# Optimization experiments

Hardware: AMD Instinct MI355X
Metric: run time of the kernel (lower is better)

The kernel has to match this reference:

```python
import jax, jax.numpy as jnp
import numpy as np

N_NODES = 50000
N_EDGES = 800000
N_GRAPHS = 1024
BN_EPS = 1e-5

def _linear_params(key, fan_in, fan_out):
    k1, k2 = jax.random.split(key)
    lim = 1.0 / np.sqrt(fan_in)
    w = jax.random.uniform(k1, (fan_in, fan_out), jnp.float32, -lim, lim)
    b = jax.random.uniform(k2, (fan_out,), jnp.float32, -lim, lim)
    return w, b


def setup_inputs() -> dict:
    key = jax.random.key(0)
    ks = jax.random.split(key, 16)
    x = jax.random.normal(ks[0], (N_NODES, 114), jnp.float32)
    edge_index = jax.random.randint(ks[1], (2, N_EDGES), 0, N_NODES, jnp.int64)
    batch = jnp.sort(jax.random.randint(ks[2], (N_NODES,), 0, N_GRAPHS, jnp.int64))
    w1a, b1a = _linear_params(ks[3], 114, 198)
    w1b, b1b = _linear_params(ks[4], 198, 198)
    w2a, b2a = _linear_params(ks[5], 198, 64)
    w2b, b2b = _linear_params(ks[6], 64, 64)
    w3a, b3a = _linear_params(ks[7], 64, 32)
    w3b, b3b = _linear_params(ks[8], 32, 32)
    fw1, fb1 = _linear_params(ks[9], 32, 16)
    fw2, fb2 = _linear_params(ks[10], 16, 8)
    ow, ob = _linear_params(ks[11], 8, 2)
    g1 = jnp.ones((198,), jnp.float32); be1 = jnp.zeros((198,), jnp.float32)
    g2 = jnp.ones((64,), jnp.float32); be2 = jnp.zeros((64,), jnp.float32)
    g3 = jnp.ones((32,), jnp.float32); be3 = jnp.zeros((32,), jnp.float32)
    return dict(x=x, edge_index=edge_index, batch=batch,
                w1a=w1a, b1a=b1a, w1b=w1b, b1b=b1b, g1=g1, be1=be1,
                w2a=w2a, b2a=b2a, w2b=w2b, b2b=b2b, g2=g2, be2=be2,
                w3a=w3a, b3a=b3a, w3b=w3b, b3b=b3b, g3=g3, be3=be3,
                fw1=fw1, fb1=fb1, fw2=fw2, fb2=fb2, ow=ow, ob=ob)


def _gin_conv(x, src, dst, wa, ba, wb, bb):
    # GINConv, eps=0: h_i = MLP((1+eps)*x_i + sum_{j->i} x_j)
    agg = jax.ops.segment_sum(x[src], dst, num_segments=N_NODES)
    h = x + agg
    h = jax.nn.relu(h @ wa + ba) @ wb + bb
    return h


def _batchnorm(h, gamma, beta):
    # training-mode BN over the node axis (biased variance, as torch)
    mean = jnp.mean(h, axis=0)
    var = jnp.var(h, axis=0)
    return (h - mean) * jax.lax.rsqrt(var + BN_EPS) * gamma + beta


def reference(x, edge_index, batch,
              w1a, b1a, w1b, b1b, g1, be1,
              w2a, b2a, w2b, b2b, g2, be2,
              w3a, b3a, w3b, b3b, g3, be3,
              fw1, fb1, fw2, fb2, ow, ob):
    src, dst = edge_index[0], edge_index[1]
    h = jax.nn.relu(_gin_conv(x, src, dst, w1a, b1a, w1b, b1b))
    h = _batchnorm(h, g1, be1)
    h = jax.nn.relu(_gin_conv(h, src, dst, w2a, b2a, w2b, b2b))
    h = _batchnorm(h, g2, be2)
    h = jax.nn.relu(_gin_conv(h, src, dst, w3a, b3a, w3b, b3b))
    h = _batchnorm(h, g3, be3)
    g = jax.ops.segment_sum(h, batch, num_segments=N_GRAPHS)  # global_add_pool
    g = jax.nn.relu(g @ fw1 + fb1)
    g = jax.nn.relu(g @ fw2 + fb2)
    return g @ ow + ob
```

## Files before the change

kernel.cpp:

```cpp
#include <hip/hip_runtime.h>

#define NODES  50000
#define EDGES  800000
#define GRAPHS 1024
#define P      200

#define SCAN_BLK 256
#define SCAN_NB  ((NODES + SCAN_BLK - 1) / SCAN_BLK)

typedef __attribute__((ext_vector_type(8))) short short8v;
typedef __attribute__((ext_vector_type(4))) short short4v;
typedef __attribute__((ext_vector_type(4))) float f32x4;

__device__ __forceinline__ ushort f2bf(float f) {
    uint u = __float_as_uint(f);
    u = u + 0x7FFFu + ((u >> 16) & 1u);
    return (ushort)(u >> 16);
}

__global__ void hist_kernel(const int* __restrict__ dst, int* __restrict__ deg) {
    int e = blockIdx.x * blockDim.x + threadIdx.x;
    if (e < EDGES) atomicAdd(&deg[dst[e]], 1);
}

__global__ void scan_part(const int* __restrict__ deg, int* __restrict__ part) {
    __shared__ int sh[SCAN_BLK];
    int t = threadIdx.x;
    int n = blockIdx.x * SCAN_BLK + t;
    sh[t] = (n < NODES) ? deg[n] : 0;
    __syncthreads();
    for (int off = SCAN_BLK / 2; off > 0; off >>= 1) {
        if (t < off) sh[t] += sh[t + off];
        __syncthreads();
    }
    if (t == 0) part[blockIdx.x] = sh[0];
}

__global__ void scan_scan(int* __restrict__ part) {
    __shared__ int sh[SCAN_BLK];
    int t = threadIdx.x;
    int v = (t < SCAN_NB) ? part[t] : 0;
    sh[t] = v;
    __syncthreads();
    for (int off = 1; off < SCAN_BLK; off <<= 1) {
        int u = 0;
        if (t >= off) u = sh[t - off];
        __syncthreads();
        if (t >= off) sh[t] += u;
        __syncthreads();
    }
    if (t < SCAN_NB) part[t] = sh[t] - v;
}

__global__ void scan_expand(const int* __restrict__ deg, const int* __restrict__ part,
                            int* __restrict__ rowstart, int* __restrict__ cursor) {
    __shared__ int sh[SCAN_BLK];
    int t = threadIdx.x;
    int n = blockIdx.x * SCAN_BLK + t;
    int v = (n < NODES) ? deg[n] : 0;
    sh[t] = v;
    __syncthreads();
    for (int off = 1; off < SCAN_BLK; off <<= 1) {
        int u = 0;
        if (t >= off) u = sh[t - off];
        __syncthreads();
        if (t >= off) sh[t] += u;
        __syncthreads();
    }
    int excl = sh[t] - v + part[blockIdx.x];
    if (n < NODES) {
        rowstart[n] = excl;
        cursor[n]   = excl;
        if (n == NODES - 1) rowstart[NODES] = excl + v;
    }
}

__global__ void scatter_kernel(const int* __restrict__ src, const int* __restrict__ dst,
                               int* __restrict__ cursor, int* __restrict__ csrc) {
    int e = blockIdx.x * blockDim.x + threadIdx.x;
    if (e < EDGES) {
        int p = atomicAdd(&cursor[dst[e]], 1);
        csrc[p] = src[e];
    }
}

__global__ void pad_w_mfma(const float* __restrict__ W, int K, int N, int NCH, int CT,
                           ushort* __restrict__ out) {
    int s = blockIdx.x * blockDim.x + threadIdx.x;
    int half = NCH * CT * 512;
    if (s >= 2 * half) return;
    int h = s / half;
    int r = s % half;
    int j = r & 7, col = (r >> 3) & 15, kg = (r >> 7) & 3;
    int rest = r >> 9;
    int ct = rest % CT, c = rest / CT;
    int k = c * 32 + kg * 8 + j;
    int n = ct * 16 + col;
    float v = (k < K && n < N) ? W[k * N + n] : 0.0f;
    ushort hi = f2bf(v);
    if (h == 0) out[s] = hi;
    else {
        float hf = __uint_as_float(((uint)hi) << 16);
        out[s] = f2bf(v - hf);
    }
}

template<int D>
__global__ void csr_agg(const float* __restrict__ feat, int fpitch,
                        const int* __restrict__ rowstart, const int* __restrict__ csrc,
                        float* __restrict__ agg, int opitch) {
    int wid  = (blockIdx.x * blockDim.x + threadIdx.x) >> 6;
    int lane = threadIdx.x & 63;
    if (wid >= NODES) return;
    constexpr int NI  = (D + 63) / 64;
    constexpr int UNR = 8;
    float s[NI];
#pragma unroll
    for (int i = 0; i < NI; i++) s[i] = 0.0f;
    const int r0 = rowstart[wid], r1 = rowstart[wid + 1];
    for (int base = r0; base < r1; base += 64) {
        const int myidx = (base + lane < r1) ? csrc[base + lane] : 0;
        const int cnt = min(64, r1 - base);
        int t = 0;
        for (; t + UNR <= cnt; t += UNR) {
            const float* p[UNR];
#pragma unroll
            for (int u = 0; u < UNR; u++)
                p[u] = feat + (size_t)__shfl(myidx, t + u) * fpitch;
            float v[UNR][NI];
#pragma unroll
            for (int u = 0; u < UNR; u++)
#pragma unroll
                for (int i = 0; i < NI; i++) {
                    int c = lane + 64 * i;
                    if (c < D) v[u][i] = p[u][c];
                }
#pragma unroll
            for (int i = 0; i < NI; i++) {
                int c = lane + 64 * i;
                if (c < D) {
                    float acc = 0.0f;
#pragma unroll
                    for (int u = 0; u < UNR; u++) acc += v[u][i];
                    s[i] += acc;
                }
            }
        }
        for (; t < cnt; t++) {
            const float* fp2 = feat + (size_t)__shfl(myidx, t) * fpitch;
#pragma unroll
            for (int i = 0; i < NI; i++) {
                int c = lane + 64 * i;
                if (c < D) s[i] += fp2[c];
            }
        }
    }
    float* ap = agg + (size_t)wid * opitch;
#pragma unroll
    for (int i = 0; i < NI; i++) {
        int c = lane + 64 * i;
        if (c < D) ap[c] = s[i];
    }
}

__launch_bounds__(256)
__global__ void gemm_fused_l1(const float* __restrict__ X,
                              const float* __restrict__ A2,
                              const ushort* __restrict__ WF1,
                              const float* __restrict__ B1,
                              const ushort* __restrict__ WF2,
                              const float* __restrict__ B2,
                              float* __restrict__ OUT,
                              float* __restrict__ gsum, float* __restrict__ gsq) {
    constexpr int K1   = 114;
    constexpr int NCH1 = 4;
    constexpr int NCH2 = 7;
    constexpr int CT   = 16;
    constexpr int CTW  = 4;
    constexpr int NN   = 198;

    __shared__ __align__(16) ushort A_lds[2][2][2][4][16][8];
    __shared__ __align__(16) ushort M_lds[2][NCH2][2][4][16][8];
    __shared__ float shSum[256];
    __shared__ float shSq [256];

    const int tid  = threadIdx.x;
    const int lane = tid & 63;
    const int wv   = tid >> 6;
    const int node0 = blockIdx.x * 32;

    for (int n = tid; n < 256; n += 256) { shSum[n] = 0.0f; shSq[n] = 0.0f; }

    const int sr  = tid >> 3;
    const int sc4 = (tid & 7) * 4;
    const int skg = sc4 >> 3;
    const int sj0 = sc4 & 7;
    const int gn  = node0 + sr;
    const size_t fstride1 = (size_t)NCH1 * CT * 512;
    const size_t fstride2 = (size_t)NCH2 * CT * 512;

    float xv[4];
    float a2v[4];

    auto loadA = [&](int c) {
        const int k0 = c * 32 + sc4;
#pragma unroll
        for (int j = 0; j < 4; j++) {
            int gk = k0 + j;
            bool ok = (gn < NODES && gk < K1);
            xv[j]  = ok ? X[(size_t)gn * K1 + gk] : 0.0f;
            a2v[j] = ok ? A2[(size_t)gn * P + gk] : 0.0f;
        }
    };
    auto cvtStore = [&](int buf, int c) {
        const int k0 = c * 32 + sc4;
        short4v hv, lv;
#pragma unroll
        for (int j = 0; j < 4; j++) {
            int gk = k0 + j;
            float t = 0.0f;
            if (gn < NODES && gk < K1) t = xv[j] + a2v[j];
            ushort h = f2bf(t);
            float hf = __uint_as_float(((uint)h) << 16);
            ushort l = f2bf(t - hf);
            hv[j] = (short)h; lv[j] = (short)l;
        }
        *(short4v*)&A_lds[buf][0][sr >> 4][skg][sr & 15][sj0] = hv;
        *(short4v*)&A_lds[buf][1][sr >> 4][skg][sr & 15][sj0] = lv;
    };

    f32x4 acc1[2][CTW] = {};
    loadA(0);
    cvtStore(0, 0);
    __syncthreads();

    const int kg = lane >> 4, rw = lane & 15;
#pragma unroll
    for (int c = 0; c < NCH1; c++) {
        const int buf = c & 1;
        if (c + 1 < NCH1) loadA(c + 1);

        short8v ah[2], al[2];
#pragma unroll
        for (int rt = 0; rt < 2; rt++) {
            ah[rt] = *(const short8v*)&A_lds[buf][0][rt][kg][rw][0];
            al[rt] = *(const short8v*)&A_lds[buf][1][rt][kg][rw][0];
        }
        const size_t fb0 = ((size_t)(c * CT + wv * CTW)) * 512 + (size_t)lane * 8;
        short8v wh = *(const short8v*)(WF1 + fb0);
        short8v wl = *(const short8v*)(WF1 + fstride1 + fb0);
#pragma unroll
        for (int t = 0; t < CTW; t++) {
            short8v nwh, nwl;
            if (t + 1 < CTW) {
                const size_t fb = fb0 + (size_t)(t + 1) * 512;
                nwh = *(const short8v*)(WF1 + fb);
                nwl = *(const short8v*)(WF1 + fstride1 + fb);
            }
            __builtin_amdgcn_s_setprio(1);
#pragma unroll
            for (int rt = 0; rt < 2; rt++) {
                acc1[rt][t] = __builtin_amdgcn_mfma_f32_16x16x32_bf16(ah[rt], wh, acc1[rt][t], 0, 0, 0);
                acc1[rt][t] = __builtin_amdgcn_mfma_f32_16x16x32_bf16(al[rt], wh, acc1[rt][t], 0, 0, 0);
                acc1[rt][t] = __builtin_amdgcn_mfma_f32_16x16x32_bf16(ah[rt], wl, acc1[rt][t], 0, 0, 0);
            }
            __builtin_amdgcn_s_setprio(0);
            if (t + 1 < CTW) { wh = nwh; wl = nwl; }
        }
        if (c + 1 < NCH1) cvtStore((c + 1) & 1, c + 1);
        __syncthreads();
    }

    const int mg = lane >> 4, colb = lane & 15;
#pragma unroll
    for (int t = 0; t < CTW; t++) {
        const int ct = wv * CTW + t;
        if (ct >= 14) continue;
        const int n = ct * 16 + colb;
        const float bn = (n < NN) ? B1[n] : 0.0f;
        const int c2 = n >> 5, kg2 = (n >> 3) & 3, j2 = n & 7;
#pragma unroll
        for (int rt = 0; rt < 2; rt++) {
#pragma unroll
            for (int j = 0; j < 4; j++) {
                float vv = fmaxf(acc1[rt][t][j] + bn, 0.0f);
                if (n >= NN) vv = 0.0f;
                ushort h = f2bf(vv);
                float hf = __uint_as_float(((uint)h) << 16);
                ushort l = f2bf(vv - hf);
                int row = mg * 4 + j;
                M_lds[0][c2][rt][kg2][row][j2] = h;
                M_lds[1][c2][rt][kg2][row][j2] = l;
            }
        }
    }
    __syncthreads();

    f32x4 acc2[2][CTW] = {};
#pragma unroll
    for (int c = 0; c < NCH2; c++) {
        short8v ah[2], al[2];
#pragma unroll
        for (int rt = 0; rt < 2; rt++) {
            ah[rt] = *(const short8v*)&M_lds[0][c][rt][kg][rw][0];
            al[rt] = *(const short8v*)&M_lds[1][c][rt][kg][rw][0];
        }
        const size_t fb0 = ((size_t)(c * CT + wv * CTW)) * 512 + (size_t)lane * 8;
        short8v wh = *(const short8v*)(WF2 + fb0);
        short8v wl = *(const short8v*)(WF2 + fstride2 + fb0);
#pragma unroll
        for (int t = 0; t < CTW; t++) {
            short8v nwh, nwl;
            if (t + 1 < CTW) {
                const size_t fb = fb0 + (size_t)(t + 1) * 512;
                nwh = *(const short8v*)(WF2 + fb);
                nwl = *(const short8v*)(WF2 + fstride2 + fb);
            }
            __builtin_amdgcn_s_setprio(1);
#pragma unroll
            for (int rt = 0; rt < 2; rt++) {
                acc2[rt][t] = __builtin_amdgcn_mfma_f32_16x16x32_bf16(ah[rt], wh, acc2[rt][t], 0, 0, 0);
                acc2[rt][t] = __builtin_amdgcn_mfma_f32_16x16x32_bf16(al[rt], wh, acc2[rt][t], 0, 0, 0);
                acc2[rt][t] = __builtin_amdgcn_mfma_f32_16x16x32_bf16(ah[rt], wl, acc2[rt][t], 0, 0, 0);
            }
            __builtin_amdgcn_s_setprio(0);
            if (t + 1 < CTW) { wh = nwh; wl = nwl; }
        }
    }

#pragma unroll
    for (int t = 0; t < CTW; t++) {
        const int ct = wv * CTW + t;
        const int n = ct * 16 + colb;
        const float bn = (n < NN) ? B2[n] : 0.0f;
        float psum = 0.0f, psq = 0.0f;
#pragma unroll
        for (int rt = 0; rt < 2; rt++) {
#pragma unroll
            for (int j = 0; j < 4; j++) {
                int m = node0 + rt * 16 + mg * 4 + j;
                float vv = fmaxf(acc2[rt][t][j] + bn, 0.0f);
                if (m < NODES && n < NN) {
                    OUT[(size_t)m * P + n] = vv;
                    psum += vv; psq += vv * vv;
                }
            }
        }
        if (n < NN) {
            atomicAdd(&shSum[n], psum);
            atomicAdd(&shSq[n], psq);
        }
    }
    __syncthreads();
    for (int n = tid; n < NN; n += 256) {
        atomicAdd(&gsum[n], shSum[n]);
        atomicAdd(&gsq[n], shSq[n]);
    }
}

template<int K, int N, bool ADD2, bool STATS, bool BNX, bool PRE, bool ACT>
__launch_bounds__(256)
__global__ void gemm_mfma(const float* __restrict__ X, int xpitch,
                          const float* __restrict__ A2, int apitch,
                          const ushort* __restrict__ WF,
                          const float* __restrict__ B,
                          const float* __restrict__ PREB,
                          const float* __restrict__ scale, const float* __restrict__ shift,
                          float* __restrict__ OUT, int opitch,
                          float* __restrict__ gsum, float* __restrict__ gsq) {
    constexpr int KP  = ((K + 31) / 32) * 32;
    constexpr int NCH = KP / 32;
    constexpr int NP  = ((N + 63) / 64) * 64;
    constexpr int CT  = NP / 16;
    constexpr int CTW = CT / 4;
    static_assert(CT % 4 == 0, "col tiles must split across 4 waves");

    __shared__ __align__(16) ushort A_lds[2][2][2][4][16][8];
    __shared__ float shSum[STATS ? NP : 4];
    __shared__ float shSq [STATS ? NP : 4];

    const int tid  = threadIdx.x;
    const int lane = tid & 63;
    const int wv   = tid >> 6;
    const int node0 = blockIdx.x * 32;

    if (STATS) {
        for (int n = tid; n < NP; n += 256) { shSum[n] = 0.0f; shSq[n] = 0.0f; }
    }

    f32x4 acc[2][CTW] = {};

    const int sr  = tid >> 3;
    const int sc4 = (tid & 7) * 4;
    const int skg = sc4 >> 3;
    const int sj0 = sc4 & 7;
    const int gn  = node0 + sr;
    const size_t fstride = (size_t)NCH * CT * 512;

    float xvA[4], xvB[4];
    float a2vA[ADD2 ? 4 : 1], a2vB[ADD2 ? 4 : 1];

    auto loadA_A = [&](int c) {
        const int k0 = c * 32 + sc4;
#pragma unroll
        for (int j = 0; j < 4; j++) {
            int gk = k0 + j;
            bool ok = (gn < NODES && gk < K);
            xvA[j] = ok ? X[(size_t)gn * xpitch + gk] : 0.0f;
            if (ADD2) a2vA[j] = ok ? A2[(size_t)gn * apitch + gk] : 0.0f;
        }
    };
    auto loadA_B = [&](int c) {
        const int k0 = c * 32 + sc4;
#pragma unroll
        for (int j = 0; j < 4; j++) {
            int gk = k0 + j;
            bool ok = (gn < NODES && gk < K);
            xvB[j] = ok ? X[(size_t)gn * xpitch + gk] : 0.0f;
            if (ADD2) a2vB[j] = ok ? A2[(size_t)gn * apitch + gk] : 0.0f;
        }
    };
    auto cvtCore = [&](int buf, int c, const float* xv, const float* a2v) {
        const int k0 = c * 32 + sc4;
        short4v hv, lv;
#pragma unroll
        for (int j = 0; j < 4; j++) {
            int gk = k0 + j;
            float t = 0.0f;
            if (gn < NODES && gk < K) {
                t = xv[j];
                if (BNX) t = fmaf(t, scale[gk], shift[gk]);
                if (ADD2) t += a2v[j];
                if (PRE)  t = fmaxf(t + PREB[gk], 0.0f);
            }
            ushort h = f2bf(t);
            float hf = __uint_as_float(((uint)h) << 16);
            ushort l = f2bf(t - hf);
            hv[j] = (short)h; lv[j] = (short)l;
        }
        *(short4v*)&A_lds[buf][0][sr >> 4][skg][sr & 15][sj0] = hv;
        *(short4v*)&A_lds[buf][1][sr >> 4][skg][sr & 15][sj0] = lv;
    };

    loadA_A(0);
    if (NCH > 1) loadA_B(1);
    cvtCore(0, 0, xvA, ADD2 ? a2vA : xvA);
    __syncthreads();

    const int kg = lane >> 4, rw = lane & 15;
#pragma unroll
    for (int c = 0; c < NCH; c++) {
        const int buf = c & 1;
        if (c + 2 < NCH) {
            if ((c & 1) == 0) loadA_A(c + 2);
            else              loadA_B(c + 2);
        }

        short8v ah[2], al[2];
#pragma unroll
        for (int rt = 0; rt < 2; rt++) {
            ah[rt] = *(const short8v*)&A_lds[buf][0][rt][kg][rw][0];
            al[rt] = *(const short8v*)&A_lds[buf][1][rt][kg][rw][0];
        }

        const size_t fb0 = ((size_t)(c * CT + wv * CTW)) * 512 + (size_t)lane * 8;
        short8v wh = *(const short8v*)(WF + fb0);
        short8v wl = *(const short8v*)(WF + fstride + fb0);
#pragma unroll
        for (int t = 0; t < CTW; t++) {
            short8v nwh, nwl;
            if (t + 1 < CTW) {
                const size_t fb = fb0 + (size_t)(t + 1) * 512;
                nwh = *(const short8v*)(WF + fb);
                nwl = *(const short8v*)(WF + fstride + fb);
            }
            __builtin_amdgcn_s_setprio(1);
#pragma unroll
            for (int rt = 0; rt < 2; rt++) {
                acc[rt][t] = __builtin_amdgcn_mfma_f32_16x16x32_bf16(ah[rt], wh, acc[rt][t], 0, 0, 0);
                acc[rt][t] = __builtin_amdgcn_mfma_f32_16x16x32_bf16(al[rt], wh, acc[rt][t], 0, 0, 0);
                acc[rt][t] = __builtin_amdgcn_mfma_f32_16x16x32_bf16(ah[rt], wl, acc[rt][t], 0, 0, 0);
            }
            __builtin_amdgcn_s_setprio(0);
            if (t + 1 < CTW) { wh = nwh; wl = nwl; }
        }

        if (c + 1 < NCH) {
            if (((c + 1) & 1) == 0) cvtCore((c + 1) & 1, c + 1, xvA, ADD2 ? a2vA : xvA);
            else                    cvtCore((c + 1) & 1, c + 1, xvB, ADD2 ? a2vB : xvB);
        }
        __syncthreads();
    }

    const int mg = lane >> 4, colb = lane & 15;
#pragma unroll
    for (int t = 0; t < CTW; t++) {
        const int ct = wv * CTW + t;
        const int n = ct * 16 + colb;
        const float bn = (ACT && n < N) ? B[n] : 0.0f;
        float psum = 0.0f, psq = 0.0f;
#pragma unroll
        for (int rt = 0; rt < 2; rt++) {
#pragma unroll
            for (int j = 0; j < 4; j++) {
                int m = node0 + rt * 16 + mg * 4 + j;
                float vv = ACT ? fmaxf(acc[rt][t][j] + bn, 0.0f) : acc[rt][t][j];
                if (m < NODES && n < N) {
                    OUT[(size_t)m * opitch + n] = vv;
                    if (STATS) { psum += vv; psq += vv * vv; }
                }
            }
        }
        if (STATS && n < N) {
            atomicAdd(&shSum[n], psum);
            atomicAdd(&shSq[n], psq);
        }
    }
    if (STATS) {
        __syncthreads();
        for (int n = tid; n < N; n += 256) {
            atomicAdd(&gsum[n], shSum[n]);
            atomicAdd(&gsq[n], shSq[n]);
        }
    }
}

template<int N>
__global__ void bn_finalize(const float* __restrict__ sum, const float* __restrict__ sq,
                            const float* __restrict__ gamma, const float* __restrict__ beta,
                            float* __restrict__ scale, float* __restrict__ shift) {
    int n = threadIdx.x;
    if (n < N) {
        float mean = sum[n] * (1.0f / NODES);
        float var  = sq[n] * (1.0f / NODES) - mean * mean;
        var = var < 0.0f ? 0.0f : var;
        float sc = gamma[n] * rsqrtf(var + 1e-5f);
        scale[n] = sc;
        shift[n] = beta[n] - mean * sc;
    }
}

__global__ void pool_kernel(const float* __restrict__ h, const int* __restrict__ batch,
                            const float* __restrict__ scale, const float* __restrict__ shift,
                            float* __restrict__ g) {
    int idx = blockIdx.x * blockDim.x + threadIdx.x;
    if (idx >= NODES * 32) return;
    int n = idx >> 5, f = idx & 31;
    float v = fmaf(h[(size_t)n * 32 + f], scale[f], shift[f]);
    atomicAdd(&g[batch[n] * 32 + f], v);
}

__global__ void head_kernel(const float* __restrict__ g,
                            const float* __restrict__ fw1, const float* __restrict__ fb1,
                            const float* __restrict__ fw2, const float* __restrict__ fb2,
                            const float* __restrict__ ow, const float* __restrict__ ob,
                            float* __restrict__ out) {
    int gi = blockIdx.x * blockDim.x + threadIdx.x;
    if (gi >= GRAPHS) return;
    float v[32];
#pragma unroll
    for (int k = 0; k < 32; k++) v[k] = g[gi * 32 + k];
    float a1[16];
#pragma unroll
    for (int o = 0; o < 16; o++) {
        float s = fb1[o];
#pragma unroll
        for (int k = 0; k < 32; k++) s = fmaf(v[k], fw1[k * 16 + o], s);
        a1[o] = s > 0.0f ? s : 0.0f;
    }
    float a2[8];
#pragma unroll
    for (int o = 0; o < 8; o++) {
        float s = fb2[o];
#pragma unroll
        for (int k = 0; k < 16; k++) s = fmaf(a1[k], fw2[k * 8 + o], s);
        a2[o] = s > 0.0f ? s : 0.0f;
    }
#pragma unroll
    for (int o = 0; o < 2; o++) {
        float s = ob[o];
#pragma unroll
        for (int k = 0; k < 8; k++) s = fmaf(a2[k], ow[k * 2 + o], s);
        out[gi * 2 + o] = s;
    }
}

extern "C" void kernel_launch(void* const* d_in, const int* in_sizes, int n_in,
                              void* d_out, int out_size, void* d_ws, size_t ws_size,
                              hipStream_t stream) {
    const float* x     = (const float*)d_in[0];
    const int*   ei    = (const int*)d_in[1];
    const int*   batch = (const int*)d_in[2];
    const float *w1a = (const float*)d_in[3],  *b1a = (const float*)d_in[4];
    const float *w1b = (const float*)d_in[5],  *b1b = (const float*)d_in[6];
    const float *g1  = (const float*)d_in[7],  *be1 = (const float*)d_in[8];
    const float *w2a = (const float*)d_in[9],  *b2a = (const float*)d_in[10];
    const float *w2b = (const float*)d_in[11], *b2b = (const float*)d_in[12];
    const float *g2  = (const float*)d_in[13], *be2 = (const float*)d_in[14];
    const float *w3a = (const float*)d_in[15], *b3a = (const float*)d_in[16];
    const float *w3b = (const float*)d_in[17], *b3b = (const float*)d_in[18];
    const float *g3  = (const float*)d_in[19], *be3 = (const float*)d_in[20];
    const float *fw1 = (const float*)d_in[21], *fb1 = (const float*)d_in[22];
    const float *fw2 = (const float*)d_in[23], *fb2 = (const float*)d_in[24];
    const float *ow  = (const float*)d_in[25], *ob  = (const float*)d_in[26];
    const int* src = ei;
    const int* dst = ei + EDGES;

    float* ws    = (float*)d_ws;
    float* b0    = ws;
    float* b1    = ws + (size_t)NODES * P;
    float* Y2    = b1;
    float* AG2   = b1 + (size_t)NODES * 64;
    float* Y3    = b1;
    float* AG3   = b1 + (size_t)NODES * 32;
    float* SUM   = ws + (size_t)2 * NODES * P;
    float* SQ    = SUM + 256;
    float* SCALE = SUM + 512;
    float* SHIFT = SUM + 768;
    float* G     = SUM + 1024;
    int*   deg      = (int*)(G + GRAPHS * 32);
    int*   rowstart = deg + NODES;
    int*   cursor   = rowstart + NODES + 1;
    int*   part     = cursor + NODES;
    int*   csrc     = part + 256;
    uintptr_t wfp = ((uintptr_t)(csrc + EDGES) + 15) & ~(uintptr_t)15;
    ushort* WF1 = (ushort*)wfp;
    ushort* WF2 = WF1 + 65536;
    ushort* WF3 = WF2 + 114688;
    ushort* WF4 = WF3 + 28672;
    ushort* WF5 = WF4 + 8192;
    ushort* WF6 = WF5 + 8192;
    float* out = (float*)d_out;

    const int GBR = (NODES + 31) / 32;
    const int AB = (NODES * 64 + 255) / 256;
    const int EB = (EDGES + 255) / 256;

    pad_w_mfma<<<(65536 + 255) / 256, 256, 0, stream>>>(w1a, 114, 198, 4, 16, WF1);
    pad_w_mfma<<<(114688 + 255) / 256, 256, 0, stream>>>(w1b, 198, 198, 7, 16, WF2);
    pad_w_mfma<<<(28672 + 255) / 256, 256, 0, stream>>>(w2a, 198, 64, 7, 4, WF3);
    pad_w_mfma<<<(8192 + 255) / 256, 256, 0, stream>>>(w2b, 64, 64, 2, 4, WF4);
    pad_w_mfma<<<(8192 + 255) / 256, 256, 0, stream>>>(w3a, 64, 32, 2, 4, WF5);
    pad_w_mfma<<<(4096 + 255) / 256, 256, 0, stream>>>(w3b, 32, 32, 1, 4, WF6);

    hipMemsetAsync(deg, 0, NODES * sizeof(int), stream);
    hist_kernel<<<EB, 256, 0, stream>>>(dst, deg);
    scan_part<<<SCAN_NB, SCAN_BLK, 0, stream>>>(deg, part);
    scan_scan<<<1, SCAN_BLK, 0, stream>>>(part);
    scan_expand<<<SCAN_NB, SCAN_BLK, 0, stream>>>(deg, part, rowstart, cursor);
    scatter_kernel<<<EB, 256, 0, stream>>>(src, dst, cursor, csrc);

    csr_agg<114><<<AB, 256, 0, stream>>>(x, 114, rowstart, csrc, b0, P);
    hipMemsetAsync(SUM, 0, 512 * sizeof(float), stream);
    gemm_fused_l1<<<GBR, 256, 0, stream>>>(x, b0, WF1, b1a, WF2, b1b, b0, SUM, SQ);
    bn_finalize<198><<<1, 256, 0, stream>>>(SUM, SQ, g1, be1, SCALE, SHIFT);

    gemm_mfma<198, 64, false, false, true, false, false><<<GBR, 256, 0, stream>>>(
        b0, P, nullptr, 0, WF3, nullptr, nullptr, SCALE, SHIFT, Y2, 64, nullptr, nullptr);
    csr_agg<64><<<AB, 256, 0, stream>>>(Y2, 64, rowstart, csrc, AG2, 64);
    hipMemsetAsync(SUM, 0, 512 * sizeof(float), stream);
    gemm_mfma<64, 64, true, true, false, true, true><<<GBR, 256, 0, stream>>>(
        Y2, 64, AG2, 64, WF4, b2b, b2a, nullptr, nullptr, b0, 64, SUM, SQ);
    bn_finalize<64><<<1, 256, 0, stream>>>(SUM, SQ, g2, be2, SCALE, SHIFT);

    gemm_mfma<64, 32, false, false, true, false, false><<<GBR, 256, 0, stream>>>(
        b0, 64, nullptr, 0, WF5, nullptr, nullptr, SCALE, SHIFT, Y3, 32, nullptr, nullptr);
    csr_agg<32><<<AB, 256, 0, stream>>>(Y3, 32, rowstart, csrc, AG3, 32);
    hipMemsetAsync(SUM, 0, 512 * sizeof(float), stream);
    gemm_mfma<32, 32, true, true, false, true, true><<<GBR, 256, 0, stream>>>(
        Y3, 32, AG3, 32, WF6, b3b, b3a, nullptr, nullptr, b0, 32, SUM, SQ);
    bn_finalize<32><<<1, 256, 0, stream>>>(SUM, SQ, g3, be3, SCALE, SHIFT);

    hipMemsetAsync(G, 0, GRAPHS * 32 * sizeof(float), stream);
    pool_kernel<<<(NODES * 32 + 255) / 256, 256, 0, stream>>>(b0, batch, SCALE, SHIFT, G);
    head_kernel<<<(GRAPHS + 255) / 256, 256, 0, stream>>>(G, fw1, fb1, fw2, fb2, ow, ob, out);
}
```

Before: 452.6 us.

## Fuse pooling into last GEMM, merge weight padding and memsets, vectorize aggregation

Global add pooling moves into the final GIN GEMM epilogue. It accumulates the raw post-ReLU activations per graph by atomics, and the head applies the BN affine algebraically using per-graph node counts computed in the histogram kernel. This removes the separate pool kernel and the write of the final layer's activations. The six weight-padding launches become one kernel, and the memsets are merged into a single contiguous zeroing with separate stat buffers per layer. The 114-wide aggregation is rewritten to use float2 loads. Per-element atomics in the GEMM epilogue may contend on graph rows.

After: 436.9 us. 1.04x faster.

```diff
diff --git a/kernel.cpp b/kernel.cpp
--- a/kernel.cpp
+++ b/kernel.cpp
@@ -18,9 +18,11 @@
     return (ushort)(u >> 16);
 }
 
-__global__ void hist_kernel(const int* __restrict__ dst, int* __restrict__ deg) {
+__global__ void hist_kernel(const int* __restrict__ dst, int* __restrict__ deg,
+                            const int* __restrict__ batch, int* __restrict__ cnt) {
     int e = blockIdx.x * blockDim.x + threadIdx.x;
     if (e < EDGES) atomicAdd(&deg[dst[e]], 1);
+    if (e < NODES) atomicAdd(&cnt[batch[e]], 1);
 }
 
 __global__ void scan_part(const int* __restrict__ deg, int* __restrict__ part) {
@@ -84,13 +86,24 @@
     }
 }
 
-__global__ void pad_w_mfma(const float* __restrict__ W, int K, int N, int NCH, int CT,
-                           ushort* __restrict__ out) {
+__global__ void pad_all(const float* __restrict__ w1a, const float* __restrict__ w1b,
+                        const float* __restrict__ w2a, const float* __restrict__ w2b,
+                        const float* __restrict__ w3a, const float* __restrict__ w3b,
+                        ushort* __restrict__ WF1, ushort* __restrict__ WF2,
+                        ushort* __restrict__ WF3, ushort* __restrict__ WF4,
+                        ushort* __restrict__ WF5, ushort* __restrict__ WF6) {
     int s = blockIdx.x * blockDim.x + threadIdx.x;
+    const float* W; ushort* out; int K, N, NCH, CT, base;
+    if      (s < 65536)  { W = w1a; out = WF1; K = 114; N = 198; NCH = 4; CT = 16; base = 0; }
+    else if (s < 180224) { W = w1b; out = WF2; K = 198; N = 198; NCH = 7; CT = 16; base = 65536; }
+    else if (s < 208896) { W = w2a; out = WF3; K = 198; N = 64;  NCH = 7; CT = 4;  base = 180224; }
+    else if (s < 217088) { W = w2b; out = WF4; K = 64;  N = 64;  NCH = 2; CT = 4;  base = 208896; }
+    else if (s < 225280) { W = w3a; out = WF5; K = 64;  N = 32;  NCH = 2; CT = 4;  base = 217088; }
+    else if (s < 229376) { W = w3b; out = WF6; K = 32;  N = 32;  NCH = 1; CT = 4;  base = 225280; }
+    else return;
+    int idx = s - base;
     int half = NCH * CT * 512;
-    if (s >= 2 * half) return;
-    int h = s / half;
-    int r = s % half;
+    int h = idx / half, r = idx % half;
     int j = r & 7, col = (r >> 3) & 15, kg = (r >> 7) & 3;
     int rest = r >> 9;
     int ct = rest % CT, c = rest / CT;
@@ -98,10 +111,10 @@
     int n = ct * 16 + col;
     float v = (k < K && n < N) ? W[k * N + n] : 0.0f;
     ushort hi = f2bf(v);
-    if (h == 0) out[s] = hi;
+    if (h == 0) out[idx] = hi;
     else {
         float hf = __uint_as_float(((uint)hi) << 16);
-        out[s] = f2bf(v - hf);
+        out[idx] = f2bf(v - hf);
     }
 }
 
@@ -112,54 +125,64 @@
     int wid  = (blockIdx.x * blockDim.x + threadIdx.x) >> 6;
     int lane = threadIdx.x & 63;
     if (wid >= NODES) return;
-    constexpr int NI  = (D + 63) / 64;
+    const int r0 = rowstart[wid], r1 = rowstart[wid + 1];
     constexpr int UNR = 8;
-    float s[NI];
-#pragma unroll
-    for (int i = 0; i < NI; i++) s[i] = 0.0f;
-    const int r0 = rowstart[wid], r1 = rowstart[wid + 1];
-    for (int base = r0; base < r1; base += 64) {
-        const int myidx = (base + lane < r1) ? csrc[base + lane] : 0;
-        const int cnt = min(64, r1 - base);
-        int t = 0;
-        for (; t + UNR <= cnt; t += UNR) {
-            const float* p[UNR];
-#pragma unroll
-            for (int u = 0; u < UNR; u++)
-                p[u] = feat + (size_t)__shfl(myidx, t + u) * fpitch;
-            float v[UNR][NI];
-#pragma unroll
-            for (int u = 0; u < UNR; u++)
-#pragma unroll
-                for (int i = 0; i < NI; i++) {
-                    int c = lane + 64 * i;
-                    if (c < D) v[u][i] = p[u][c];
+    if constexpr (D == 114) {
+        const bool act = lane < 57;
+        float sx = 0.0f, sy = 0.0f;
+        for (int base = r0; base < r1; base += 64) {
+            const int myidx = (base + lane < r1) ? csrc[base + lane] : 0;
+            const int cnt = min(64, r1 - base);
+            int t = 0;
+            for (; t + UNR <= cnt; t += UNR) {
+                const float2* p[UNR];
+#pragma unroll
+                for (int u = 0; u < UNR; u++)
+                    p[u] = (const float2*)(feat + (size_t)__shfl(myidx, t + u) * fpitch);
+                float2 v[UNR];
+#pragma unroll
+                for (int u = 0; u < UNR; u++) if (act) v[u] = p[u][lane];
+                if (act) {
+                    float ax = 0.0f, ay = 0.0f;
+#pragma unroll
+                    for (int u = 0; u < UNR; u++) { ax += v[u].x; ay += v[u].y; }
+                    sx += ax; sy += ay;
                 }
-#pragma unroll
-            for (int i = 0; i < NI; i++) {
-                int c = lane + 64 * i;
-                if (c < D) {
+            }
+            for (; t < cnt; t++) {
+                const float2* fp2 = (const float2*)(feat + (size_t)__shfl(myidx, t) * fpitch);
+                if (act) { float2 v = fp2[lane]; sx += v.x; sy += v.y; }
+            }
+        }
+        if (act) *(float2*)(agg + (size_t)wid * opitch + 2 * lane) = make_float2(sx, sy);
+    } else {
+        float s = 0.0f;
+        for (int base = r0; base < r1; base += 64) {
+            const int myidx = (base + lane < r1) ? csrc[base + lane] : 0;
+            const int cnt = min(64, r1 - base);
+            int t = 0;
+            for (; t + UNR <= cnt; t += UNR) {
+                const float* p[UNR];
+#pragma unroll
+                for (int u = 0; u < UNR; u++)
+                    p[u] = feat + (size_t)__shfl(myidx, t + u) * fpitch;
+                float v[UNR];
+#pragma unroll
+                for (int u = 0; u < UNR; u++)
+                    if (lane < D) v[u] = p[u][lane];
+                if (lane < D) {
                     float acc = 0.0f;
 #pragma unroll
-                    for (int u = 0; u < UNR; u++) acc += v[u][i];
-                    s[i] += acc;
+                    for (int u = 0; u < UNR; u++) acc += v[u];
+                    s += acc;
                 }
             }
-        }
-        for (; t < cnt; t++) {
-            const float* fp2 = feat + (size_t)__shfl(myidx, t) * fpitch;
-#pragma unroll
-            for (int i = 0; i < NI; i++) {
-                int c = lane + 64 * i;
-                if (c < D) s[i] += fp2[c];
-            }
-        }
-    }
-    float* ap = agg + (size_t)wid * opitch;
-#pragma unroll
-    for (int i = 0; i < NI; i++) {
-        int c = lane + 64 * i;
-        if (c < D) ap[c] = s[i];
+            for (; t < cnt; t++) {
+                const float* fp2 = feat + (size_t)__shfl(myidx, t) * fpitch;
+                if (lane < D) s += fp2[lane];
+            }
+        }
+        if (lane < D) agg[(size_t)wid * opitch + lane] = s;
     }
 }
 
@@ -358,7 +381,8 @@
     }
 }
 
-template<int K, int N, bool ADD2, bool STATS, bool BNX, bool PRE, bool ACT>
+template<int K, int N, bool ADD2, bool STATS, bool BNX, bool PRE, bool ACT,
+         bool WRITE, bool POOL>
 __launch_bounds__(256)
 __global__ void gemm_mfma(const float* __restrict__ X, int xpitch,
                           const float* __restrict__ A2, int apitch,
@@ -367,7 +391,8 @@
                           const float* __restrict__ PREB,
                           const float* __restrict__ scale, const float* __restrict__ shift,
                           float* __restrict__ OUT, int opitch,
-                          float* __restrict__ gsum, float* __restrict__ gsq) {
+                          float* __restrict__ gsum, float* __restrict__ gsq,
+                          const int* __restrict__ batch, float* __restrict__ gpool) {
     constexpr int KP  = ((K + 31) / 32) * 32;
     constexpr int NCH = KP / 32;
     constexpr int NP  = ((N + 63) / 64) * 64;
@@ -506,8 +531,9 @@
                 int m = node0 + rt * 16 + mg * 4 + j;
                 float vv = ACT ? fmaxf(acc[rt][t][j] + bn, 0.0f) : acc[rt][t][j];
                 if (m < NODES && n < N) {
-                    OUT[(size_t)m * opitch + n] = vv;
+                    if (WRITE) OUT[(size_t)m * opitch + n] = vv;
                     if (STATS) { psum += vv; psq += vv * vv; }
+                    if (POOL)  atomicAdd(&gpool[batch[m] * 32 + n], vv);
                 }
             }
         }
@@ -540,26 +566,19 @@
     }
 }
 
-__global__ void pool_kernel(const float* __restrict__ h, const int* __restrict__ batch,
+__global__ void head_kernel(const float* __restrict__ graw, const int* __restrict__ cnt,
                             const float* __restrict__ scale, const float* __restrict__ shift,
-                            float* __restrict__ g) {
-    int idx = blockIdx.x * blockDim.x + threadIdx.x;
-    if (idx >= NODES * 32) return;
-    int n = idx >> 5, f = idx & 31;
-    float v = fmaf(h[(size_t)n * 32 + f], scale[f], shift[f]);
-    atomicAdd(&g[batch[n] * 32 + f], v);
-}
-
-__global__ void head_kernel(const float* __restrict__ g,
                             const float* __restrict__ fw1, const float* __restrict__ fb1,
                             const float* __restrict__ fw2, const float* __restrict__ fb2,
                             const float* __restrict__ ow, const float* __restrict__ ob,
                             float* __restrict__ out) {
     int gi = blockIdx.x * blockDim.x + threadIdx.x;
     if (gi >= GRAPHS) return;
+    float cf = (float)cnt[gi];
     float v[32];
 #pragma unroll
-    for (int k = 0; k < 32; k++) v[k] = g[gi * 32 + k];
+    for (int k = 0; k < 32; k++)
+        v[k] = fmaf(graw[gi * 32 + k], scale[k], cf * shift[k]);
     float a1[16];
 #pragma unroll
     for (int o = 0; o < 16; o++) {
@@ -606,23 +625,31 @@
     const int* src = ei;
     const int* dst = ei + EDGES;
 
-    float* ws    = (float*)d_ws;
-    float* b0    = ws;
-    float* b1    = ws + (size_t)NODES * P;
-    float* Y2    = b1;
-    float* AG2   = b1 + (size_t)NODES * 64;
-    float* Y3    = b1;
-    float* AG3   = b1 + (size_t)NODES * 32;
-    float* SUM   = ws + (size_t)2 * NODES * P;
-    float* SQ    = SUM + 256;
-    float* SCALE = SUM + 512;
-    float* SHIFT = SUM + 768;
-    float* G     = SUM + 1024;
-    int*   deg      = (int*)(G + GRAPHS * 32);
-    int*   rowstart = deg + NODES;
-    int*   cursor   = rowstart + NODES + 1;
-    int*   part     = cursor + NODES;
-    int*   csrc     = part + 256;
+    float* ws  = (float*)d_ws;
+    float* b0  = ws;
+    float* b1  = ws + (size_t)NODES * P;
+    float* Y2  = b1;
+    float* AG2 = b1 + (size_t)NODES * 64;
+    float* Y3  = b1;
+    float* AG3 = b1 + (size_t)NODES * 32;
+
+    int*   deg  = (int*)(ws + (size_t)2 * NODES * P);
+    int*   cnt  = deg + NODES;
+    float* SUM1 = (float*)(cnt + GRAPHS);
+    float* SQ1  = SUM1 + 256;
+    float* SUM2 = SQ1 + 256;
+    float* SQ2  = SUM2 + 256;
+    float* SUM3 = SQ2 + 256;
+    float* SQ3  = SUM3 + 256;
+    float* G    = SQ3 + 256;
+    const size_t ZERO_ELEMS = (size_t)NODES + GRAPHS + 6 * 256 + (size_t)GRAPHS * 32;
+
+    float* SCALE = G + (size_t)GRAPHS * 32;
+    float* SHIFT = SCALE + 256;
+    int* rowstart = (int*)(SHIFT + 256);
+    int* cursor   = rowstart + NODES + 1;
+    int* part     = cursor + NODES;
+    int* csrc     = part + 256;
     uintptr_t wfp = ((uintptr_t)(csrc + EDGES) + 15) & ~(uintptr_t)15;
     ushort* WF1 = (ushort*)wfp;
     ushort* WF2 = WF1 + 65536;
@@ -636,42 +663,38 @@
     const int AB = (NODES * 64 + 255) / 256;
     const int EB = (EDGES + 255) / 256;
 
-    pad_w_mfma<<<(65536 + 255) / 256, 256, 0, stream>>>(w1a, 114, 198, 4, 16, WF1);
-    pad_w_mfma<<<(114688 + 255) / 256, 256, 0, stream>>>(w1b, 198, 198, 7, 16, WF2);
-    pad_w_mfma<<<(28672 + 255) / 256, 256, 0, stream>>>(w2a, 198, 64, 7, 4, WF3);
-    pad_w_mfma<<<(8192 + 255) / 256, 256, 0, stream>>>(w2b, 64, 64, 2, 4, WF4);
-    pad_w_mfma<<<(8192 + 255) / 256, 256, 0, stream>>>(w3a, 64, 32, 2, 4, WF5);
-    pad_w_mfma<<<(4096 + 255) / 256, 256, 0, stream>>>(w3b, 32, 32, 1, 4, WF6);
-
-    hipMemsetAsync(deg, 0, NODES * sizeof(int), stream);
-    hist_kernel<<<EB, 256, 0, stream>>>(dst, deg);
+    pad_all<<<(229376 + 255) / 256, 256, 0, stream>>>(w1a, w1b, w2a, w2b, w3a, w3b,
+                                                      WF1, WF2, WF3, WF4, WF5, WF6);
+    hipMemsetAsync(deg, 0, ZERO_ELEMS * sizeof(int), stream);
+
+    hist_kernel<<<EB, 256, 0, stream>>>(dst, deg, batch, cnt);
     scan_part<<<SCAN_NB, SCAN_BLK, 0, stream>>>(deg, part);
     scan_scan<<<1, SCAN_BLK, 0, stream>>>(part);
     scan_expand<<<SCAN_NB, SCAN_BLK, 0, stream>>>(deg, part, rowstart, cursor);
     scatter_kernel<<<EB, 256, 0, stream>>>(src, dst, cursor, csrc);
 
     csr_agg<114><<<AB, 256, 0, stream>>>(x, 114, rowstart, csrc, b0, P);
-    hipMemsetAsync(SUM, 0, 512 * sizeof(float), stream);
-    gemm_fused_l1<<<GBR, 256, 0, stream>>>(x, b0, WF1, b1a, WF2, b1b, b0, SUM, SQ);
-    bn_finalize<198><<<1, 256, 0, stream>>>(SUM, SQ, g1, be1, SCALE, SHIFT);
-
-    gemm_mfma<198, 64, false, false, true, false, false><<<GBR, 256, 0, stream>>>(
-        b0, P, nullptr, 0, WF3, nullptr, nullptr, SCALE, SHIFT, Y2, 64, nullptr, nullptr);
+    gemm_fused_l1<<<GBR, 256, 0, stream>>>(x, b0, WF1, b1a, WF2, b1b, b0, SUM1, SQ1);
+    bn_finalize<198><<<1, 256, 0, stream>>>(SUM1, SQ1, g1, be1, SCALE, SHIFT);
+
+    gemm_mfma<198, 64, false, false, true, false, false, true, false><<<GBR, 256, 0, stream>>>(
+        b0, P, nullptr, 0, WF3, nullptr, nullptr, SCALE, SHIFT, Y2, 64, nullptr, nullptr,
+        nullptr, nullptr);
     csr_agg<64><<<AB, 256, 0, stream>>>(Y2, 64, rowstart, csrc, AG2, 64);
-    hipMemsetAsync(SUM, 0, 512 * sizeof(float), stream);
-    gemm_mfma<64, 64, true, true, false, true, true><<<GBR, 256, 0, stream>>>(
-        Y2, 64, AG2, 64, WF4, b2b, b2a, nullptr, nullptr, b0, 64, SUM, SQ);
-    bn_finalize<64><<<1, 256, 0, stream>>>(SUM, SQ, g2, be2, SCALE, SHIFT);
-
-    gemm_mfma<64, 32, false, false, true, false, false><<<GBR, 256, 0, stream>>>(
-        b0, 64, nullptr, 0, WF5, nullptr, nullptr, SCALE, SHIFT, Y3, 32, nullptr, nullptr);
+    gemm_mfma<64, 64, true, true, false, true, true, true, false><<<GBR, 256, 0, stream>>>(
+        Y2, 64, AG2, 64, WF4, b2b, b2a, nullptr, nullptr, b0, 64, SUM2, SQ2,
+        nullptr, nullptr);
+    bn_finalize<64><<<1, 256, 0, stream>>>(SUM2, SQ2, g2, be2, SCALE, SHIFT);
+
+    gemm_mfma<64, 32, false, false, true, false, false, true, false><<<GBR, 256, 0, stream>>>(
+        b0, 64, nullptr, 0, WF5, nullptr, nullptr, SCALE, SHIFT, Y3, 32, nullptr, nullptr,
+        nullptr, nullptr);
     csr_agg<32><<<AB, 256, 0, stream>>>(Y3, 32, rowstart, csrc, AG3, 32);
-    hipMemsetAsync(SUM, 0, 512 * sizeof(float), stream);
-    gemm_mfma<32, 32, true, true, false, true, true><<<GBR, 256, 0, stream>>>(
-        Y3, 32, AG3, 32, WF6, b3b, b3a, nullptr, nullptr, b0, 32, SUM, SQ);
-    bn_finalize<32><<<1, 256, 0, stream>>>(SUM, SQ, g3, be3, SCALE, SHIFT);
-
-    hipMemsetAsync(G, 0, GRAPHS * 32 * sizeof(float), stream);
-    pool_kernel<<<(NODES * 32 + 255) / 256, 256, 0, stream>>>(b0, batch, SCALE, SHIFT, G);
-    head_kernel<<<(GRAPHS + 255) / 256, 256, 0, stream>>>(G, fw1, fb1, fw2, fb2, ow, ob, out);
-}
+    gemm_mfma<32, 32, true, true, false, true, true, false, true><<<GBR, 256, 0, stream>>>(
+        Y3, 32, AG3, 32, WF6, b3b, b3a, nullptr, nullptr, nullptr, 32, SUM3, SQ3,
+        batch, G);
+    bn_finalize<32><<<1, 256, 0, stream>>>(SUM3, SQ3, g3, be3, SCALE, SHIFT);
+
+    head_kernel<<<(GRAPHS + 255) / 256, 256, 0, stream>>>(
+        G, cnt, SCALE, SHIFT, fw1, fb1, fw2, fb2, ow, ob, out);
+}
```
